# Optimization experiments

Measured on AMD Instinct MI355X. Metric: run time of the kernel, lower is better.

Reference implementation:

```python
import jax, jax.numpy as jnp
import numpy as np

N = 100_000   # nodes
E = 600_000   # edges
D = 128       # embed_dim
G = 1000      # graphs (batch ids)
L = 3         # num_layers


def setup_inputs() -> dict:
    key = jax.random.key(0)
    ks = jax.random.split(key, 12)
    s = 1.0 / np.sqrt(D)
    return {
        "x": jax.random.normal(ks[0], (N, D), jnp.float32),
        "edge_index": jax.random.randint(ks[1], (2, E), 0, N),
        "batch": jnp.sort(jax.random.randint(ks[2], (N,), 0, G)),
        "mask": jax.random.randint(ks[3], (N,), 0, 2),
        # stacked GCNConv weights/biases (in=hidden=out=D)
        "gcn_w": jax.random.normal(ks[4], (L, D, D), jnp.float32) * s,
        "gcn_b": jnp.zeros((L, D), jnp.float32),
        # MLP head: Linear(D,D) -> ReLU -> Linear(D,1)
        "lin1_w": jax.random.normal(ks[5], (D, D), jnp.float32) * s,
        "lin1_b": jnp.zeros((D,), jnp.float32),
        "lin2_w": jax.random.normal(ks[6], (D,), jnp.float32) * s,
        "lin2_b": jnp.zeros((), jnp.float32),
    }


def gcn_forward(x, src, dst, gcn_w, gcn_b):
    # symmetric gcn_norm with self-loops: deg[i] = 1 + in-degree(i)
    deg = jax.ops.segment_sum(jnp.ones((E,), x.dtype), dst, num_segments=N) + 1.0
    dinv = jax.lax.rsqrt(deg)
    enorm = dinv[src] * dinv[dst]          # [E] edge normalization
    self_norm = (dinv * dinv)[:, None]     # [N,1] self-loop normalization
    h = x
    for l in range(L):
        h = h @ gcn_w[l]                   # [N,D]
        h = (jax.ops.segment_sum(h[src] * enorm[:, None], dst, num_segments=N)
             + h * self_norm)
        h = h + gcn_b[l]
        if l < L - 1:
            h = jax.nn.relu(h)  # (dropout inactive at inference)
    return h


def reference(x, edge_index, batch, mask, gcn_w, gcn_b, lin1_w, lin1_b, lin2_w, lin2_b):
    src, dst = edge_index[0], edge_index[1]
    h = gcn_forward(x, src, dst, gcn_w, gcn_b)
    # MLP head -> per-node score [N]
    s = jax.nn.relu(h @ lin1_w + lin1_b) @ lin2_w + lin2_b
    s = jnp.where(mask == 0, jnp.float32(-1e9), s)
    # per-graph (segment) softmax — fused replacement for the unique/batch loop
    m = jax.ops.segment_max(s, batch, num_segments=G)
    e = jnp.exp(s - m[batch])
    z = jax.ops.segment_sum(e, batch, num_segments=G)
    return e / z[batch]
```

## Files before the change

kernel.cpp:

```cpp
#include <hip/hip_runtime.h>
#include <hip/hip_bf16.h>

typedef unsigned int u32;
typedef unsigned short u16;
typedef __attribute__((ext_vector_type(8))) short bf16x8;
typedef __attribute__((ext_vector_type(4))) float f32x4;

__device__ __forceinline__ float u16tof(u16 u){ return __uint_as_float(((u32)u) << 16); }
__device__ __forceinline__ float lo16(u32 v){ return __uint_as_float(v << 16); }
__device__ __forceinline__ float hi16(u32 v){ return __uint_as_float(v & 0xffff0000u); }
__device__ __forceinline__ u16 ftobf(float f){
  u32 b = __float_as_uint(f);
  return (u16)((b + 0x7FFFu + ((b >> 16) & 1u)) >> 16);
}
__device__ __forceinline__ u32 pack2(float a, float b){
  return (u32)ftobf(a) | ((u32)ftobf(b) << 16);
}
__device__ __forceinline__ float ldf(const void* p, int i, int isbf){
  return isbf ? u16tof(((const u16*)p)[i]) : ((const float*)p)[i];
}

__global__ __launch_bounds__(256) void k_prep(const void* __restrict__ gw, const void* __restrict__ l1w,
                                              const void* __restrict__ x, u16* __restrict__ Wf,
                                              u16* __restrict__ Hb, int L, int n8, int cvtB, int goffB,
                                              const int* __restrict__ batch, int* __restrict__ goff,
                                              int N, int G,
                                              const int* __restrict__ dst, int* __restrict__ bcnt,
                                              int nE, int chunk, int* __restrict__ flag){
  __shared__ int sh[256];
  const int b = blockIdx.x;
  const int t = threadIdx.x;
  const int histStart = L + 1 + cvtB + goffB;

  if (b >= histStart){
    sh[t] = 0; __syncthreads();
    const int blk = b - histStart;
    const int e0 = blk * chunk, e1 = min(e0 + chunk, nE);
    for (int e = e0 + t; e < e1; e += 256) atomicAdd(&sh[dst[e] >> 9], 1);
    __syncthreads();
    if (sh[t] > 0) atomicAdd(&bcnt[t], sh[t]);
    return;
  }
  if (b >= L + 1 + cvtB){
    const int i = (b - (L + 1 + cvtB)) * 256 + t;
    if (i >= N) return;
    const int bt = batch[i];
    const int prev = (i == 0) ? -1 : batch[i - 1];
    for (int g = prev + 1; g <= bt; ++g) goff[g] = i;
    if (i == N - 1){ for (int g = bt + 1; g <= G; ++g) goff[g] = N; }
    return;
  }
  if (t == 0) sh[0] = 0;
  __syncthreads();
  if (b <= L){
    int local = 0;
    for (int i = t; i < 4096; i += 256){
      u32 e = (((const u32*)gw)[i] >> 7) & 0xFFu;
      if (e >= 100u && e < 127u) local++;
    }
    atomicAdd(&sh[0], local);
    __syncthreads();
    const int isbf = (sh[0] > 2048) ? 1 : 0;
    if (b == 0 && t == 0) *flag = isbf;

    const void* src = (b < L) ? gw : l1w;
    const int sbase = (b < L) ? b * 16384 : 0;
    u16* dstp = Wf + (size_t)b * 16384;
    for (int g = t; g < 2048; g += 256){
      const int tt = g >> 8, ks = (g >> 6) & 3, lane = g & 63;
      const int n = tt * 16 + (lane & 15);
      const int k0 = ks * 32 + ((lane >> 4) << 3);
      u16* d = dstp + (size_t)g * 8;
      #pragma unroll
      for (int j = 0; j < 8; ++j){
        d[j] = ftobf(ldf(src, sbase + (k0 + j) * 128 + n, isbf));
      }
    }
  } else {
    u32 e = (((const u32*)gw)[t] >> 7) & 0xFFu;
    atomicAdd(&sh[0], (e >= 100u && e < 127u) ? 1 : 0);
    __syncthreads();
    if (sh[0] > 128) return;
    const int i = (b - (L + 1)) * 256 + t;
    if (i >= n8) return;
    const float4 a = ((const float4*)x)[i * 2];
    const float4 c = ((const float4*)x)[i * 2 + 1];
    u16* o = Hb + (size_t)i * 8;
    o[0] = ftobf(a.x); o[1] = ftobf(a.y); o[2] = ftobf(a.z); o[3] = ftobf(a.w);
    o[4] = ftobf(c.x); o[5] = ftobf(c.y); o[6] = ftobf(c.z); o[7] = ftobf(c.w);
  }
}

__global__ __launch_bounds__(256) void k_scatter(const int* __restrict__ src, const int* __restrict__ dst,
                                                 const int* __restrict__ bcnt, int* __restrict__ bpos0,
                                                 int2* __restrict__ tmpe, int nE, int chunk){
  __shared__ int sm[256];
  __shared__ int cnt[256];
  __shared__ int base[256];
  const int blk = blockIdx.x, t = threadIdx.x;
  const int v = bcnt[t];
  sm[t] = v;
  cnt[t] = 0;
  __syncthreads();
  for (int off = 1; off < 256; off <<= 1){
    int a = (t >= off) ? sm[t - off] : 0;
    __syncthreads();
    sm[t] += a;
    __syncthreads();
  }
  const int ex = sm[t] - v;
  const int e0 = blk * chunk, e1 = min(e0 + chunk, nE);
  for (int e = e0 + t; e < e1; e += 256) atomicAdd(&cnt[dst[e] >> 9], 1);
  __syncthreads();
  if (cnt[t] > 0) base[t] = ex + atomicAdd(&bpos0[t], cnt[t]);
  __syncthreads();
  for (int e = e0 + t; e < e1; e += 256){
    const int d = dst[e];
    const int pos = atomicAdd(&base[d >> 9], 1);
    tmpe[pos] = make_int2(src[e], d);
  }
}

__global__ __launch_bounds__(256) void k_local(const int2* __restrict__ tmpe, const int* __restrict__ bcnt,
                                               int* __restrict__ boff, int* __restrict__ eid,
                                               float* __restrict__ dinv, int N, int nE, int nbkt){
  __shared__ int sm[256];
  __shared__ int hcnt[512];
  __shared__ int hoff[512];
  const int b = blockIdx.x, t = threadIdx.x;
  sm[t] = bcnt[t];
  __syncthreads();
  for (int off = 1; off < 256; off <<= 1){
    int a = (t >= off) ? sm[t - off] : 0;
    __syncthreads();
    sm[t] += a;
    __syncthreads();
  }
  const int e0 = (b == 0) ? 0 : sm[b - 1];
  const int e1 = sm[b];
  const int n0 = b << 9;
  const int n1 = min(n0 + 512, N);
  const int nn = n1 - n0;
  hcnt[t] = 0; hcnt[t + 256] = 0;
  __syncthreads();
  for (int e = e0 + t; e < e1; e += 256) atomicAdd(&hcnt[tmpe[e].y - n0], 1);
  __syncthreads();
  const int v0 = hcnt[t], v1 = hcnt[t + 256];
  hoff[t] = v0; hoff[t + 256] = v1;
  __syncthreads();
  for (int off = 1; off < 512; off <<= 1){
    int a0 = (t >= off) ? hoff[t - off] : 0;
    int a1 = (t + 256 >= off) ? hoff[t + 256 - off] : 0;
    __syncthreads();
    hoff[t] += a0; hoff[t + 256] += a1;
    __syncthreads();
  }
  const int ex0 = hoff[t] - v0 + e0;
  const int ex1 = hoff[t + 256] - v1 + e0;
  if (t < nn){       boff[n0 + t] = ex0;        dinv[n0 + t] = rsqrtf((float)v0 + 1.0f); }
  if (t + 256 < nn){ boff[n0 + t + 256] = ex1;  dinv[n0 + t + 256] = rsqrtf((float)v1 + 1.0f); }
  if (b == nbkt - 1 && t == 0) boff[N] = nE;
  __syncthreads();
  hoff[t] = ex0; hoff[t + 256] = ex1;
  __syncthreads();
  for (int e = e0 + t; e < e1; e += 256){
    const int2 pr = tmpe[e];
    const int pos = atomicAdd(&hoff[pr.y - n0], 1);
    eid[pos] = pr.x;
  }
}

__global__ __launch_bounds__(256) void k_mm(const void* __restrict__ X, const u16* __restrict__ Hb,
                                            const u16* __restrict__ Wf, const float* __restrict__ dinv,
                                            u16* __restrict__ T, int n, const int* __restrict__ fl){
  __shared__ u16 smw[16384];
  const int isbf = *fl;
  const u16* A = isbf ? (const u16*)X : Hb;
  {
    const uint4* s = (const uint4*)Wf;
    uint4* d = (uint4*)smw;
    for (int i = threadIdx.x; i < 2048; i += 256) d[i] = s[i];
  }
  __syncthreads();

  const int wave = threadIdx.x >> 6, lane = threadIdx.x & 63;
  const int m0 = blockIdx.x * 64 + wave * 16;
  int arow = m0 + (lane & 15); if (arow > n - 1) arow = n - 1;
  const u16* aptr = A + (size_t)arow * 128 + ((lane >> 4) << 3);

  f32x4 acc[8];
  #pragma unroll
  for (int t = 0; t < 8; ++t) acc[t] = (f32x4){0.f, 0.f, 0.f, 0.f};

  #pragma unroll
  for (int ks = 0; ks < 4; ++ks){
    const bf16x8 a = *(const bf16x8*)(aptr + ks * 32);
    #pragma unroll
    for (int t = 0; t < 8; ++t){
      const bf16x8 b = *(const bf16x8*)(smw + (size_t)(((t * 4 + ks) * 64 + lane) * 8));
      acc[t] = __builtin_amdgcn_mfma_f32_16x16x32_bf16(a, b, acc[t], 0, 0, 0);
    }
  }
  __syncthreads();

  const int quad = lane >> 4, col0 = lane & 15;
  float dv[4];
  #pragma unroll
  for (int r = 0; r < 4; ++r){
    const int row = m0 + quad * 4 + r;
    dv[r] = (row < n) ? dinv[row] : 0.f;
  }
  u16* my = smw + wave * 2112;
  #pragma unroll
  for (int t = 0; t < 8; ++t){
    #pragma unroll
    for (int r = 0; r < 4; ++r){
      my[(quad * 4 + r) * 132 + t * 16 + col0] = ftobf(acc[t][r] * dv[r]);
    }
  }
  #pragma unroll
  for (int i = 0; i < 4; ++i){
    const int row = i * 4 + (lane >> 4);
    const int grow = m0 + row;
    const int c8 = (lane & 15) * 8;
    if (grow < n){
      const u16* s = &my[row * 132 + c8];
      uint2 lo = *(const uint2*)(s);
      uint2 hi = *(const uint2*)(s + 4);
      *(uint4*)&T[(size_t)grow * 128 + c8] = make_uint4(lo.x, lo.y, hi.x, hi.y);
    }
  }
}

__global__ __launch_bounds__(256) void k_gmm(const u16* __restrict__ Tin, const int* __restrict__ boff,
                                             const int* __restrict__ eid, const float* __restrict__ dinv,
                                             const void* __restrict__ bias, int layer,
                                             const u16* __restrict__ Wf, u16* __restrict__ Tout,
                                             int n, const int* __restrict__ fl){
  __shared__ u16 smw[16384];
  __shared__ u16 sma[16 * 132];
  const int isbf = *fl;
  const int wave = threadIdx.x >> 6, lane = threadIdx.x & 63;
  const int sub = lane >> 4, l16 = lane & 15;
  const int m0 = blockIdx.x * 16;

  {
    const uint4* s = (const uint4*)Wf;
    uint4* d = (uint4*)smw;
    for (int i = threadIdx.x; i < 2048; i += 256) d[i] = s[i];
  }

  const int node = m0 + wave * 4 + sub;
  float h0=0,h1=0,h2=0,h3=0,h4=0,h5=0,h6=0,h7=0;
  if (node < n){
    const uint4 sv = ((const uint4*)(Tin + (size_t)node * 128))[l16];
    float a0 = lo16(sv.x), a1 = hi16(sv.x), a2 = lo16(sv.y), a3 = hi16(sv.y);
    float a4 = lo16(sv.z), a5 = hi16(sv.z), a6 = lo16(sv.w), a7 = hi16(sv.w);
    int j = boff[node];
    const int b1e = boff[node + 1];
    for (; j + 4 <= b1e; j += 4){
      const int s0 = eid[j], s1 = eid[j + 1], s2 = eid[j + 2], s3 = eid[j + 3];
      const uint4 v0 = ((const uint4*)(Tin + (size_t)s0 * 128))[l16];
      const uint4 v1 = ((const uint4*)(Tin + (size_t)s1 * 128))[l16];
      const uint4 v2 = ((const uint4*)(Tin + (size_t)s2 * 128))[l16];
      const uint4 v3 = ((const uint4*)(Tin + (size_t)s3 * 128))[l16];
      a0 += (lo16(v0.x) + lo16(v1.x)) + (lo16(v2.x) + lo16(v3.x));
      a1 += (hi16(v0.x) + hi16(v1.x)) + (hi16(v2.x) + hi16(v3.x));
      a2 += (lo16(v0.y) + lo16(v1.y)) + (lo16(v2.y) + lo16(v3.y));
      a3 += (hi16(v0.y) + hi16(v1.y)) + (hi16(v2.y) + hi16(v3.y));
      a4 += (lo16(v0.z) + lo16(v1.z)) + (lo16(v2.z) + lo16(v3.z));
      a5 += (hi16(v0.z) + hi16(v1.z)) + (hi16(v2.z) + hi16(v3.z));
      a6 += (lo16(v0.w) + lo16(v1.w)) + (lo16(v2.w) + lo16(v3.w));
      a7 += (hi16(v0.w) + hi16(v1.w)) + (hi16(v2.w) + hi16(v3.w));
    }
    for (; j < b1e; ++j){
      const uint4 v = ((const uint4*)(Tin + (size_t)eid[j] * 128))[l16];
      a0 += lo16(v.x); a1 += hi16(v.x);
      a2 += lo16(v.y); a3 += hi16(v.y);
      a4 += lo16(v.z); a5 += hi16(v.z);
      a6 += lo16(v.w); a7 += hi16(v.w);
    }
    const float di = dinv[node];
    const int bb = layer * 128 + l16 * 8;
    h0 = fmaxf(fmaf(a0, di, ldf(bias, bb + 0, isbf)), 0.f);
    h1 = fmaxf(fmaf(a1, di, ldf(bias, bb + 1, isbf)), 0.f);
    h2 = fmaxf(fmaf(a2, di, ldf(bias, bb + 2, isbf)), 0.f);
    h3 = fmaxf(fmaf(a3, di, ldf(bias, bb + 3, isbf)), 0.f);
    h4 = fmaxf(fmaf(a4, di, ldf(bias, bb + 4, isbf)), 0.f);
    h5 = fmaxf(fmaf(a5, di, ldf(bias, bb + 5, isbf)), 0.f);
    h6 = fmaxf(fmaf(a6, di, ldf(bias, bb + 6, isbf)), 0.f);
    h7 = fmaxf(fmaf(a7, di, ldf(bias, bb + 7, isbf)), 0.f);
  }
  {
    uint4 o;
    o.x = pack2(h0, h1); o.y = pack2(h2, h3); o.z = pack2(h4, h5); o.w = pack2(h6, h7);
    *(uint4*)&sma[(wave * 4 + sub) * 132 + l16 * 8] = o;
  }
  __syncthreads();

  f32x4 acc[2];
  acc[0] = (f32x4){0.f,0.f,0.f,0.f}; acc[1] = (f32x4){0.f,0.f,0.f,0.f};
  #pragma unroll
  for (int ks = 0; ks < 4; ++ks){
    const bf16x8 a = *(const bf16x8*)(sma + l16 * 132 + sub * 8 + ks * 32);
    #pragma unroll
    for (int tt = 0; tt < 2; ++tt){
      const int t = wave * 2 + tt;
      const bf16x8 b = *(const bf16x8*)(smw + (size_t)(((t * 4 + ks) * 64 + lane) * 8));
      acc[tt] = __builtin_amdgcn_mfma_f32_16x16x32_bf16(a, b, acc[tt], 0, 0, 0);
    }
  }
  __syncthreads();

  float dv[4];
  #pragma unroll
  for (int r = 0; r < 4; ++r){
    const int row = m0 + sub * 4 + r;
    dv[r] = (row < n) ? dinv[row] : 0.f;
  }
  #pragma unroll
  for (int tt = 0; tt < 2; ++tt){
    const int t = wave * 2 + tt;
    #pragma unroll
    for (int r = 0; r < 4; ++r){
      sma[(sub * 4 + r) * 132 + t * 16 + l16] = ftobf(acc[tt][r] * dv[r]);
    }
  }
  __syncthreads();

  {
    const int row = threadIdx.x >> 4;
    const int c8 = (threadIdx.x & 15) * 8;
    if (m0 + row < n){
      const u16* s = &sma[row * 132 + c8];
      uint2 lo = *(const uint2*)(s);
      uint2 hi = *(const uint2*)(s + 4);
      *(uint4*)&Tout[(size_t)(m0 + row) * 128 + c8] = make_uint4(lo.x, lo.y, hi.x, hi.y);
    }
  }
}

__global__ __launch_bounds__(256) void k_ghead(const u16* __restrict__ Tin, const int* __restrict__ boff,
                                               const int* __restrict__ eid, const float* __restrict__ dinv,
                                               const void* __restrict__ bias, int layer,
                                               const u16* __restrict__ Wf, const void* __restrict__ b1,
                                               const void* __restrict__ w2, const void* __restrict__ b2,
                                               const int* __restrict__ mask, float* __restrict__ s,
                                               int n, const int* __restrict__ fl){
  __shared__ u16 smw[16384];
  __shared__ u16 sma[16 * 132];
  __shared__ float sred[4][16];
  const int isbf = *fl;
  const int wave = threadIdx.x >> 6, lane = threadIdx.x & 63;
  const int sub = lane >> 4, l16 = lane & 15;
  const int m0 = blockIdx.x * 16;

  {
    const uint4* sp = (const uint4*)Wf;
    uint4* d = (uint4*)smw;
    for (int i = threadIdx.x; i < 2048; i += 256) d[i] = sp[i];
  }

  const int node = m0 + wave * 4 + sub;
  float h0=0,h1=0,h2=0,h3=0,h4=0,h5=0,h6=0,h7=0;
  if (node < n){
    const uint4 sv = ((const uint4*)(Tin + (size_t)node * 128))[l16];
    float a0 = lo16(sv.x), a1 = hi16(sv.x), a2 = lo16(sv.y), a3 = hi16(sv.y);
    float a4 = lo16(sv.z), a5 = hi16(sv.z), a6 = lo16(sv.w), a7 = hi16(sv.w);
    int j = boff[node];
    const int b1e = boff[node + 1];
    for (; j + 4 <= b1e; j += 4){
      const int s0 = eid[j], s1 = eid[j + 1], s2 = eid[j + 2], s3 = eid[j + 3];
      const uint4 v0 = ((const uint4*)(Tin + (size_t)s0 * 128))[l16];
      const uint4 v1 = ((const uint4*)(Tin + (size_t)s1 * 128))[l16];
      const uint4 v2 = ((const uint4*)(Tin + (size_t)s2 * 128))[l16];
      const uint4 v3 = ((const uint4*)(Tin + (size_t)s3 * 128))[l16];
      a0 += (lo16(v0.x) + lo16(v1.x)) + (lo16(v2.x) + lo16(v3.x));
      a1 += (hi16(v0.x) + hi16(v1.x)) + (hi16(v2.x) + hi16(v3.x));
      a2 += (lo16(v0.y) + lo16(v1.y)) + (lo16(v2.y) + lo16(v3.y));
      a3 += (hi16(v0.y) + hi16(v1.y)) + (hi16(v2.y) + hi16(v3.y));
      a4 += (lo16(v0.z) + lo16(v1.z)) + (lo16(v2.z) + lo16(v3.z));
      a5 += (hi16(v0.z) + hi16(v1.z)) + (hi16(v2.z) + hi16(v3.z));
      a6 += (lo16(v0.w) + lo16(v1.w)) + (lo16(v2.w) + lo16(v3.w));
      a7 += (hi16(v0.w) + hi16(v1.w)) + (hi16(v2.w) + hi16(v3.w));
    }
    for (; j < b1e; ++j){
      const uint4 v = ((const uint4*)(Tin + (size_t)eid[j] * 128))[l16];
      a0 += lo16(v.x); a1 += hi16(v.x);
      a2 += lo16(v.y); a3 += hi16(v.y);
      a4 += lo16(v.z); a5 += hi16(v.z);
      a6 += lo16(v.w); a7 += hi16(v.w);
    }
    const float di = dinv[node];
    const int bb = layer * 128 + l16 * 8;
    h0 = fmaf(a0, di, ldf(bias, bb + 0, isbf));
    h1 = fmaf(a1, di, ldf(bias, bb + 1, isbf));
    h2 = fmaf(a2, di, ldf(bias, bb + 2, isbf));
    h3 = fmaf(a3, di, ldf(bias, bb + 3, isbf));
    h4 = fmaf(a4, di, ldf(bias, bb + 4, isbf));
    h5 = fmaf(a5, di, ldf(bias, bb + 5, isbf));
    h6 = fmaf(a6, di, ldf(bias, bb + 6, isbf));
    h7 = fmaf(a7, di, ldf(bias, bb + 7, isbf));
  }
  {
    uint4 o;
    o.x = pack2(h0, h1); o.y = pack2(h2, h3); o.z = pack2(h4, h5); o.w = pack2(h6, h7);
    *(uint4*)&sma[(wave * 4 + sub) * 132 + l16 * 8] = o;
  }
  __syncthreads();

  f32x4 acc[2];
  acc[0] = (f32x4){0.f,0.f,0.f,0.f}; acc[1] = (f32x4){0.f,0.f,0.f,0.f};
  #pragma unroll
  for (int ks = 0; ks < 4; ++ks){
    const bf16x8 a = *(const bf16x8*)(sma + l16 * 132 + sub * 8 + ks * 32);
    #pragma unroll
    for (int tt = 0; tt < 2; ++tt){
      const int t = wave * 2 + tt;
      const bf16x8 b = *(const bf16x8*)(smw + (size_t)(((t * 4 + ks) * 64 + lane) * 8));
      acc[tt] = __builtin_amdgcn_mfma_f32_16x16x32_bf16(a, b, acc[tt], 0, 0, 0);
    }
  }

  float p0 = 0.f, p1 = 0.f, p2 = 0.f, p3 = 0.f;
  #pragma unroll
  for (int tt = 0; tt < 2; ++tt){
    const int col = (wave * 2 + tt) * 16 + l16;
    const float bv = ldf(b1, col, isbf);
    const float wv = ldf(w2, col, isbf);
    p0 = fmaf(fmaxf(acc[tt][0] + bv, 0.f), wv, p0);
    p1 = fmaf(fmaxf(acc[tt][1] + bv, 0.f), wv, p1);
    p2 = fmaf(fmaxf(acc[tt][2] + bv, 0.f), wv, p2);
    p3 = fmaf(fmaxf(acc[tt][3] + bv, 0.f), wv, p3);
  }
  #pragma unroll
  for (int k = 1; k < 16; k <<= 1){
    p0 += __shfl_xor(p0, k);
    p1 += __shfl_xor(p1, k);
    p2 += __shfl_xor(p2, k);
    p3 += __shfl_xor(p3, k);
  }
  if (l16 == 0){
    sred[wave][sub * 4 + 0] = p0;
    sred[wave][sub * 4 + 1] = p1;
    sred[wave][sub * 4 + 2] = p2;
    sred[wave][sub * 4 + 3] = p3;
  }
  __syncthreads();
  if (threadIdx.x < 16){
    const int row = m0 + threadIdx.x;
    if (row < n){
      float sc = sred[0][threadIdx.x] + sred[1][threadIdx.x] + sred[2][threadIdx.x] + sred[3][threadIdx.x]
               + ldf(b2, 0, isbf);
      if (mask[row] == 0) sc = -1e9f;
      s[row] = sc;
    }
  }
}

__global__ __launch_bounds__(256) void k_gsm(const float* __restrict__ s, const int* __restrict__ goff,
                                             void* __restrict__ out, int G, const int* __restrict__ fl){
  const int g = blockIdx.x * 4 + (threadIdx.x >> 6);
  if (g >= G) return;
  const int lane = threadIdx.x & 63;
  const int i0 = goff[g], i1 = goff[g + 1];
  if (i0 >= i1) return;
  float m = -3.4e38f;
  for (int j = i0 + lane; j < i1; j += 64) m = fmaxf(m, s[j]);
  #pragma unroll
  for (int k = 32; k; k >>= 1) m = fmaxf(m, __shfl_xor(m, k));
  float zz = 0.f;
  for (int j = i0 + lane; j < i1; j += 64) zz += expf(s[j] - m);
  #pragma unroll
  for (int k = 32; k; k >>= 1) zz += __shfl_xor(zz, k);
  const float rz = 1.f / zz;
  const int isbf = *fl;
  for (int j = i0 + lane; j < i1; j += 64){
    const float v = expf(s[j] - m) * rz;
    if (isbf) ((u16*)out)[j] = ftobf(v);
    else      ((float*)out)[j] = v;
  }
}

extern "C" void kernel_launch(void* const* d_in, const int* in_sizes, int n_in,
                              void* d_out, int out_size, void* d_ws, size_t ws_size,
                              hipStream_t stream){
  const void* x    = d_in[0];
  const int* ei    = (const int*)d_in[1];
  const int* batch = (const int*)d_in[2];
  const int* mask  = (const int*)d_in[3];
  const void* gw   = d_in[4];
  const void* gb   = d_in[5];
  const void* l1w  = d_in[6];
  const void* l1b  = d_in[7];
  const void* l2w  = d_in[8];
  const void* l2b  = d_in[9];

  const int N = in_sizes[2];
  const int E = in_sizes[1] / 2;
  const int D = 128;
  const int L = in_sizes[4] / (D * D);
  const int G = 1000;

  char* p = (char*)d_ws;
  u16*  Hb    = (u16*)p;   p += (size_t)N * D * sizeof(u16);
  u16*  Tb    = (u16*)p;   p += (size_t)N * D * sizeof(u16);
  u16*  Wf    = (u16*)p;   p += (size_t)(L + 1) * D * D * sizeof(u16);
  float* dinv = (float*)p; p += (size_t)N * sizeof(float);
  float* sbuf = (float*)p; p += (size_t)N * sizeof(float);
  int*  boff  = (int*)p;   p += (size_t)(N + 1) * sizeof(int);
  int*  eid   = (int*)p;   p += (size_t)E * sizeof(int);
  int*  goff  = (int*)p;   p += (size_t)(G + 1) * sizeof(int);
  int*  bcnt  = (int*)p;   p += 256 * sizeof(int);
  int*  bpos0 = (int*)p;   p += 256 * sizeof(int);
  int2* tmpe  = (int2*)p;  p += (size_t)E * sizeof(int2);
  int*  flag  = (int*)p;   p += 256;

  const int* srcp = ei;
  const int* dstp = ei + E;

  const int mmg   = (N + 63) / 64;
  const int fg    = (N + 15) / 16;
  const int n8    = N * D / 8;
  const int cvtB  = (n8 + 255) / 256;
  const int goffB = (N + 255) / 256;
  const int chunk = (E + 255) / 256;
  const int nbkt  = (N + 511) / 512;

  hipMemsetAsync(bcnt, 0, 512 * sizeof(int), stream);

  k_prep<<<(L + 1) + cvtB + goffB + 256, 256, 0, stream>>>(gw, l1w, x, Wf, Hb, L, n8, cvtB, goffB,
                                                           batch, goff, N, G, dstp, bcnt, E, chunk, flag);
  k_scatter<<<256, 256, 0, stream>>>(srcp, dstp, bcnt, bpos0, tmpe, E, chunk);
  k_local<<<nbkt, 256, 0, stream>>>(tmpe, bcnt, boff, eid, dinv, N, E, nbkt);

  k_mm<<<mmg, 256, 0, stream>>>(x, Hb, Wf, dinv, Tb, N, flag);
  k_gmm<<<fg, 256, 0, stream>>>(Tb, boff, eid, dinv, gb, 0, Wf + (size_t)1 * D * D, Hb, N, flag);
  k_gmm<<<fg, 256, 0, stream>>>(Hb, boff, eid, dinv, gb, 1, Wf + (size_t)2 * D * D, Tb, N, flag);
  k_ghead<<<fg, 256, 0, stream>>>(Tb, boff, eid, dinv, gb, 2, Wf + (size_t)L * D * D,
                                  l1b, l2w, l2b, mask, sbuf, N, flag);
  k_gsm<<<(G + 3) / 4, 256, 0, stream>>>(sbuf, goff, d_out, G, flag);
}
```

Measured before the change: 357.7 us.

## Replace atomic bucket counts with per-block histogram scan; read weights from global in gmm

The edge bucketing now writes a per-block histogram from k_prep, and a new single-block k_hscan kernel computes exclusive per-block offsets and bucket bases. This removes the memset, the repeated 256-wide scans in k_scatter and k_local, and the second dst histogram pass in k_scatter. Separately, k_gmm and k_ghead no longer stage the 32KB weight matrix into shared memory and instead load B fragments straight from global/L2. That cuts LDS use and raises occupancy, at the cost of more global loads per MFMA and one extra small serial kernel launch.

```diff
diff --git a/kernel.cpp b/kernel.cpp
--- a/kernel.cpp
+++ b/kernel.cpp
@@ -25,7 +25,7 @@
                                               u16* __restrict__ Hb, int L, int n8, int cvtB, int goffB,
                                               const int* __restrict__ batch, int* __restrict__ goff,
                                               int N, int G,
-                                              const int* __restrict__ dst, int* __restrict__ bcnt,
+                                              const int* __restrict__ dst, int* __restrict__ hist,
                                               int nE, int chunk, int* __restrict__ flag){
   __shared__ int sh[256];
   const int b = blockIdx.x;
@@ -38,7 +38,7 @@
     const int e0 = blk * chunk, e1 = min(e0 + chunk, nE);
     for (int e = e0 + t; e < e1; e += 256) atomicAdd(&sh[dst[e] >> 9], 1);
     __syncthreads();
-    if (sh[t] > 0) atomicAdd(&bcnt[t], sh[t]);
+    hist[blk * 256 + t] = sh[t];
     return;
   }
   if (b >= L + 1 + cvtB){
@@ -91,29 +91,34 @@
   }
 }
 
+__global__ __launch_bounds__(256) void k_hscan(int* __restrict__ hist, int* __restrict__ bb, int nE){
+  const int t = threadIdx.x;
+  int run = 0;
+  for (int j = 0; j < 256; ++j){
+    const int v = hist[j * 256 + t];
+    hist[j * 256 + t] = run;
+    run += v;
+  }
+  __shared__ int sm[256];
+  sm[t] = run; __syncthreads();
+  for (int off = 1; off < 256; off <<= 1){
+    int a = (t >= off) ? sm[t - off] : 0;
+    __syncthreads();
+    sm[t] += a;
+    __syncthreads();
+  }
+  bb[t] = sm[t] - run;
+  if (t == 255) bb[256] = nE;
+}
+
 __global__ __launch_bounds__(256) void k_scatter(const int* __restrict__ src, const int* __restrict__ dst,
-                                                 const int* __restrict__ bcnt, int* __restrict__ bpos0,
+                                                 const int* __restrict__ hist, const int* __restrict__ bb,
                                                  int2* __restrict__ tmpe, int nE, int chunk){
-  __shared__ int sm[256];
-  __shared__ int cnt[256];
   __shared__ int base[256];
   const int blk = blockIdx.x, t = threadIdx.x;
-  const int v = bcnt[t];
-  sm[t] = v;
-  cnt[t] = 0;
-  __syncthreads();
-  for (int off = 1; off < 256; off <<= 1){
-    int a = (t >= off) ? sm[t - off] : 0;
-    __syncthreads();
-    sm[t] += a;
-    __syncthreads();
-  }
-  const int ex = sm[t] - v;
+  base[t] = bb[t] + hist[blk * 256 + t];
+  __syncthreads();
   const int e0 = blk * chunk, e1 = min(e0 + chunk, nE);
-  for (int e = e0 + t; e < e1; e += 256) atomicAdd(&cnt[dst[e] >> 9], 1);
-  __syncthreads();
-  if (cnt[t] > 0) base[t] = ex + atomicAdd(&bpos0[t], cnt[t]);
-  __syncthreads();
   for (int e = e0 + t; e < e1; e += 256){
     const int d = dst[e];
     const int pos = atomicAdd(&base[d >> 9], 1);
@@ -121,26 +126,16 @@
   }
 }
 
-__global__ __launch_bounds__(256) void k_local(const int2* __restrict__ tmpe, const int* __restrict__ bcnt,
+__global__ __launch_bounds__(256) void k_local(const int2* __restrict__ tmpe, const int* __restrict__ bb,
                                                int* __restrict__ boff, int* __restrict__ eid,
                                                float* __restrict__ dinv, int N, int nE, int nbkt){
-  __shared__ int sm[256];
   __shared__ int hcnt[512];
   __shared__ int hoff[512];
   const int b = blockIdx.x, t = threadIdx.x;
-  sm[t] = bcnt[t];
-  __syncthreads();
-  for (int off = 1; off < 256; off <<= 1){
-    int a = (t >= off) ? sm[t - off] : 0;
-    __syncthreads();
-    sm[t] += a;
-    __syncthreads();
-  }
-  const int e0 = (b == 0) ? 0 : sm[b - 1];
-  const int e1 = sm[b];
   const int n0 = b << 9;
   const int n1 = min(n0 + 512, N);
   const int nn = n1 - n0;
+  const int e0 = bb[b], e1 = bb[b + 1];
   hcnt[t] = 0; hcnt[t + 256] = 0;
   __syncthreads();
   for (int e = e0 + t; e < e1; e += 256) atomicAdd(&hcnt[tmpe[e].y - n0], 1);
@@ -237,18 +232,11 @@
                                              const void* __restrict__ bias, int layer,
                                              const u16* __restrict__ Wf, u16* __restrict__ Tout,
                                              int n, const int* __restrict__ fl){
-  __shared__ u16 smw[16384];
   __shared__ u16 sma[16 * 132];
   const int isbf = *fl;
   const int wave = threadIdx.x >> 6, lane = threadIdx.x & 63;
   const int sub = lane >> 4, l16 = lane & 15;
   const int m0 = blockIdx.x * 16;
-
-  {
-    const uint4* s = (const uint4*)Wf;
-    uint4* d = (uint4*)smw;
-    for (int i = threadIdx.x; i < 2048; i += 256) d[i] = s[i];
-  }
 
   const int node = m0 + wave * 4 + sub;
   float h0=0,h1=0,h2=0,h3=0,h4=0,h5=0,h6=0,h7=0;
@@ -306,7 +294,7 @@
     #pragma unroll
     for (int tt = 0; tt < 2; ++tt){
       const int t = wave * 2 + tt;
-      const bf16x8 b = *(const bf16x8*)(smw + (size_t)(((t * 4 + ks) * 64 + lane) * 8));
+      const bf16x8 b = *(const bf16x8*)(Wf + (size_t)(((t * 4 + ks) * 64 + lane) * 8));
       acc[tt] = __builtin_amdgcn_mfma_f32_16x16x32_bf16(a, b, acc[tt], 0, 0, 0);
     }
   }
@@ -347,19 +335,12 @@
                                                const void* __restrict__ w2, const void* __restrict__ b2,
                                                const int* __restrict__ mask, float* __restrict__ s,
                                                int n, const int* __restrict__ fl){
-  __shared__ u16 smw[16384];
   __shared__ u16 sma[16 * 132];
   __shared__ float sred[4][16];
   const int isbf = *fl;
   const int wave = threadIdx.x >> 6, lane = threadIdx.x & 63;
   const int sub = lane >> 4, l16 = lane & 15;
   const int m0 = blockIdx.x * 16;
-
-  {
-    const uint4* sp = (const uint4*)Wf;
-    uint4* d = (uint4*)smw;
-    for (int i = threadIdx.x; i < 2048; i += 256) d[i] = sp[i];
-  }
 
   const int node = m0 + wave * 4 + sub;
   float h0=0,h1=0,h2=0,h3=0,h4=0,h5=0,h6=0,h7=0;
@@ -417,7 +398,7 @@
     #pragma unroll
     for (int tt = 0; tt < 2; ++tt){
       const int t = wave * 2 + tt;
-      const bf16x8 b = *(const bf16x8*)(smw + (size_t)(((t * 4 + ks) * 64 + lane) * 8));
+      const bf16x8 b = *(const bf16x8*)(Wf + (size_t)(((t * 4 + ks) * 64 + lane) * 8));
       acc[tt] = __builtin_amdgcn_mfma_f32_16x16x32_bf16(a, b, acc[tt], 0, 0, 0);
     }
   }
@@ -511,8 +492,8 @@
   int*  boff  = (int*)p;   p += (size_t)(N + 1) * sizeof(int);
   int*  eid   = (int*)p;   p += (size_t)E * sizeof(int);
   int*  goff  = (int*)p;   p += (size_t)(G + 1) * sizeof(int);
-  int*  bcnt  = (int*)p;   p += 256 * sizeof(int);
-  int*  bpos0 = (int*)p;   p += 256 * sizeof(int);
+  int*  hist  = (int*)p;   p += 256 * 256 * sizeof(int);
+  int*  bb    = (int*)p;   p += 260 * sizeof(int);
   int2* tmpe  = (int2*)p;  p += (size_t)E * sizeof(int2);
   int*  flag  = (int*)p;   p += 256;
 
@@ -527,12 +508,11 @@
   const int chunk = (E + 255) / 256;
   const int nbkt  = (N + 511) / 512;
 
-  hipMemsetAsync(bcnt, 0, 512 * sizeof(int), stream);
-
   k_prep<<<(L + 1) + cvtB + goffB + 256, 256, 0, stream>>>(gw, l1w, x, Wf, Hb, L, n8, cvtB, goffB,
-                                                           batch, goff, N, G, dstp, bcnt, E, chunk, flag);
-  k_scatter<<<256, 256, 0, stream>>>(srcp, dstp, bcnt, bpos0, tmpe, E, chunk);
-  k_local<<<nbkt, 256, 0, stream>>>(tmpe, bcnt, boff, eid, dinv, N, E, nbkt);
+                                                           batch, goff, N, G, dstp, hist, E, chunk, flag);
+  k_hscan<<<1, 256, 0, stream>>>(hist, bb, E);
+  k_scatter<<<256, 256, 0, stream>>>(srcp, dstp, hist, bb, tmpe, E, chunk);
+  k_local<<<nbkt, 256, 0, stream>>>(tmpe, bb, boff, eid, dinv, N, E, nbkt);
 
   k_mm<<<mmg, 256, 0, stream>>>(x, Hb, Wf, dinv, Tb, N, flag);
   k_gmm<<<fg, 256, 0, stream>>>(Tb, boff, eid, dinv, gb, 0, Wf + (size_t)1 * D * D, Hb, N, flag);
```

After: 320.7 us (median of 2 runs). -10.4%, faster.
